# Performance work log

Measured on AMD Instinct MI355X. Metric: run time of the kernel, lower is better.

## Reference

```python
import jax, jax.numpy as jnp
import numpy as np

KERNEL_MUL = 2.0
KERNEL_NUM = 5


def _mmd(source, target):
    b = source.shape[0]
    total = jnp.concatenate([source, target], axis=0)  # [2N, D]
    # ||a-b||^2 = ||a||^2 + ||b||^2 - 2 a.b  (GEMM form, avoids [2N,2N,D])
    sq = jnp.sum(total * total, axis=1)  # [2N]
    l2 = sq[:, None] + sq[None, :] - 2.0 * (total @ total.T)  # [2N, 2N]
    n = total.shape[0]
    # bandwidth computed on detached distances (torch uses .data)
    bandwidth = jax.lax.stop_gradient(jnp.sum(l2)) / (n * n - n)
    kernels = sum(jnp.exp(-l2 / (bandwidth * KERNEL_MUL ** i)) for i in range(KERNEL_NUM))
    xx = kernels[:b, :b]
    yy = kernels[b:, b:]
    xy = kernels[:b, b:]
    yx = kernels[b:, :b]
    return jnp.mean(xx + yy - xy - yx)


def setup_inputs() -> dict:
    key = jax.random.key(0)
    k1, k2 = jax.random.split(key)
    source = jax.random.normal(k1, (4096, 512), dtype=jnp.float32)
    target = jax.random.normal(k2, (4096, 512), dtype=jnp.float32)
    return {"source": source, "target": target}


def reference(source, target):
    return _mmd(source, target)
```

## Files before the change

### kernel.cpp

```cpp
#include <hip/hip_runtime.h>
#include <stdint.h>

typedef signed char s8;
typedef int i32x4 __attribute__((ext_vector_type(4)));

#define B_HALF 4096
#define NROWS 8192
#define DCOL 512
#define BM 128
#define TT 64
#define NTILES 2080
#define KT 8
#define QSCALE 32.0f
#define INV_S2 (1.0f / 1024.0f)
#define PREP_BLOCKS (NROWS / 16)
#define NREP 8

__global__ void zero_kernel(uint4* __restrict__ p) {
  int t = threadIdx.x;
#pragma unroll
  for (int i = 0; i < 5; ++i)
    p[t + i * 256] = (uint4){0u, 0u, 0u, 0u};
}

__global__ __launch_bounds__(256) void prep_kernel(const float* __restrict__ src,
    const float* __restrict__ tgt, s8* __restrict__ qp,
    float* __restrict__ sqq, float* __restrict__ colsum_rep,
    double* __restrict__ sumsq_rep, unsigned int* __restrict__ counter,
    float* __restrict__ gf_out) {
  __shared__ float cs[4][DCOL];
  __shared__ double redd[4];
  __shared__ int lastFlag;
  int tid = threadIdx.x;
  int lane = tid & 63, wid = tid >> 6;
  float cpart[8] = {0.f,0.f,0.f,0.f,0.f,0.f,0.f,0.f};
  float myssq = 0.f;
  int row0 = blockIdx.x * 16;
#pragma unroll
  for (int r = 0; r < 4; ++r) {
    int row = row0 + r * 4 + wid;
    const float* x = (row < B_HALF) ? (src + (size_t)row * DCOL)
                                    : (tgt + (size_t)(row - B_HALF) * DCOL);
    float4 v0 = *reinterpret_cast<const float4*>(x + lane * 8);
    float4 v1 = *reinterpret_cast<const float4*>(x + lane * 8 + 4);
    float vals[8] = {v0.x, v0.y, v0.z, v0.w, v1.x, v1.y, v1.z, v1.w};
    union { s8 c[8]; uint2 u; } pu;
    int iq = 0;
#pragma unroll
    for (int q = 0; q < 8; ++q) {
      float f = vals[q];
      myssq += f * f;
      cpart[q] += f;
      int k = __float2int_rn(fminf(fmaxf(f * QSCALE, -127.f), 127.f));
      pu.c[q] = (s8)k;
      iq += k * k;
    }
    *reinterpret_cast<uint2*>(qp + (size_t)row * DCOL + lane * 8) = pu.u;
#pragma unroll
    for (int o = 32; o > 0; o >>= 1) iq += __shfl_down(iq, o);
    if (lane == 0) sqq[row] = (float)iq * INV_S2;
  }
  double dssq = (double)myssq;
#pragma unroll
  for (int o = 32; o > 0; o >>= 1) dssq += __shfl_down(dssq, o);
  if (lane == 0) redd[wid] = dssq;
#pragma unroll
  for (int q = 0; q < 8; ++q) cs[wid][lane * 8 + q] = cpart[q];
  __syncthreads();
  int rep = (blockIdx.x & (NREP - 1)) * DCOL;
  int c = tid;
  atomicAdd(&colsum_rep[rep + c],
            cs[0][c] + cs[1][c] + cs[2][c] + cs[3][c]);
  atomicAdd(&colsum_rep[rep + c + 256],
            cs[0][c + 256] + cs[1][c + 256] + cs[2][c + 256] + cs[3][c + 256]);
  if (tid == 0)
    atomicAdd(&sumsq_rep[blockIdx.x & (NREP - 1)],
              redd[0] + redd[1] + redd[2] + redd[3]);

  asm volatile("s_waitcnt vmcnt(0)" ::: "memory");
  __syncthreads();
  if (tid == 0)
    lastFlag = ((atomicAdd(counter, 1u) % (unsigned)PREP_BLOCKS) == PREP_BLOCKS - 1);
  __syncthreads();
  if (lastFlag) {
    float c0 = 0.f, c1 = 0.f;
#pragma unroll
    for (int r = 0; r < NREP; ++r) {
      c0 += atomicAdd(&colsum_rep[r * DCOL + tid], 0.f);
      c1 += atomicAdd(&colsum_rep[r * DCOL + tid + 256], 0.f);
    }
    double scs = (double)c0 * c0 + (double)c1 * c1;
#pragma unroll
    for (int o = 32; o > 0; o >>= 1) scs += __shfl_down(scs, o);
    if (lane == 0) redd[wid] = scs;
    __syncthreads();
    if (tid == 0) {
      double C2 = redd[0] + redd[1] + redd[2] + redd[3];
      double S = 0.0;
#pragma unroll
      for (int r = 0; r < NREP; ++r) S += atomicAdd(&sumsq_rep[r], 0.0);
      double n = (double)NROWS;
      double bwv = (2.0 * n * S - 2.0 * C2) / (n * n - n);
      gf_out[0] = (float)(-1.0 / (16.0 * bwv));
    }
  }
}

#define GLDS(gptr, lptr) __builtin_amdgcn_global_load_lds( \
    (const __attribute__((address_space(1))) void*)(gptr), \
    (__attribute__((address_space(3))) void*)(lptr), 16, 0, 0)

#define STAGE(KT_, BUF_) do { \
    GLDS(gA0 + (size_t)(KT_) * 64,             &qA[BUF_][wid * 2048]); \
    GLDS(gA0 + (size_t)(KT_) * 64 + 16 * DCOL, &qA[BUF_][wid * 2048 + 1024]); \
    GLDS(gB0 + (size_t)(KT_) * 64,             &qB[BUF_][wid * 2048]); \
    GLDS(gB0 + (size_t)(KT_) * 64 + 16 * DCOL, &qB[BUF_][wid * 2048 + 1024]); \
  } while (0)

__global__ __launch_bounds__(256, 3) void mmd_gemm_kernel(
    const s8* __restrict__ qp, const float* __restrict__ sqq,
    const float* __restrict__ gf_ptr, float* __restrict__ partials) {
  __shared__ __align__(16) s8 qA[3][8192];
  __shared__ __align__(16) s8 qB[3][8192];
  __shared__ float sqR[BM], sqC[BM];

  int bid = blockIdx.x;
  int t6 = (bid & 7) * (NTILES / 8) + (bid >> 3);
  int I = 0, rem = t6;
  while (rem >= TT - I) { rem -= TT - I; ++I; }
  int J = I + rem;
  int rowStart = I * BM, colStart = J * BM;

  int tid = threadIdx.x;
  int lane = tid & 63, wid = tid >> 6;
  int wr = wid >> 1, wc = wid & 1;
  int r15 = lane & 15, kg = lane >> 4;

  int u = (lane & 7) ^ (lane >> 3);
  int drow0 = wid * 16 + (lane >> 3);
  const s8* gA0 = qp + (size_t)(rowStart + drow0 * 2 + (u >> 2)) * DCOL + (u & 3) * 16;
  const s8* gB0 = qp + (size_t)(colStart + drow0 * 2 + (u >> 2)) * DCOL + (u & 3) * 16;

  int laneOff = ((r15 >> 1) * 128) +
                (((((r15 & 1) << 2) | kg) ^ ((r15 >> 1) & 7)) << 4);
  int aBase = wr * 4096 + laneOff;
  int bBase = wc * 4096 + laneOff;

  STAGE(0, 0);
  STAGE(1, 1);
  if (tid < BM) sqR[tid] = sqq[rowStart + tid];
  else          sqC[tid - BM] = sqq[colStart + (tid - BM)];
  float gf = gf_ptr[0];
  asm volatile("s_waitcnt vmcnt(4) lgkmcnt(0)" ::: "memory");
  __builtin_amdgcn_s_barrier();

  i32x4 acc[4][4];
#pragma unroll
  for (int m = 0; m < 4; ++m)
#pragma unroll
    for (int n = 0; n < 4; ++n) acc[m][n] = (i32x4){0, 0, 0, 0};

#pragma unroll
  for (int kt = 0; kt < KT; ++kt) {
    const int buf = kt % 3;

    i32x4 a[4], b[4];
#pragma unroll
    for (int m = 0; m < 4; ++m)
      a[m] = *reinterpret_cast<const i32x4*>(&qA[buf][aBase + m * 1024]);
#pragma unroll
    for (int n = 0; n < 4; ++n)
      b[n] = *reinterpret_cast<const i32x4*>(&qB[buf][bBase + n * 1024]);

    if (kt + 2 < KT) STAGE(kt + 2, (kt + 2) % 3);

#pragma unroll
    for (int m = 0; m < 4; ++m)
#pragma unroll
      for (int n = 0; n < 4; ++n)
        acc[m][n] = __builtin_amdgcn_mfma_i32_16x16x64_i8(a[m], b[n], acc[m][n], 0, 0, 0);

    if (kt + 2 < KT) {
      asm volatile("s_waitcnt vmcnt(4)" ::: "memory");
      __builtin_amdgcn_s_barrier();
    } else if (kt + 1 < KT) {
      asm volatile("s_waitcnt vmcnt(0)" ::: "memory");
      __builtin_amdgcn_s_barrier();
    }
  }

  float partial = 0.f;
  int rbase = (lane >> 4) * 4;
#pragma unroll
  for (int m = 0; m < 4; ++m) {
    float sr[4];
#pragma unroll
    for (int e = 0; e < 4; ++e) sr[e] = sqR[wr * 64 + m * 16 + rbase + e];
#pragma unroll
    for (int n = 0; n < 4; ++n) {
      float sc = sqC[wc * 64 + n * 16 + r15];
#pragma unroll
      for (int e = 0; e < 4; ++e) {
        float d = (float)acc[m][n][e] * INV_S2;
        float l2v = sr[e] + sc - 2.f * d;
        float uu = __expf(gf * l2v);
        float u2 = uu * uu, u4 = u2 * u2, u8 = u4 * u4, u16v = u8 * u8;
        partial += uu + u2 + u4 + u8 + u16v;
      }
    }
  }
  float wsign = ((I == J) ? 1.f : 2.f) *
                (((rowStart < B_HALF) == (colStart < B_HALF)) ? 1.f : -1.f);
  partial *= wsign;
#pragma unroll
  for (int o = 32; o > 0; o >>= 1) partial += __shfl_down(partial, o);
  if (lane == 0) partials[bid * 4 + wid] = partial;
}

__global__ void finalize_kernel(const float* __restrict__ partials,
                                float* __restrict__ out) {
  __shared__ double red[256];
  int tid = threadIdx.x;
  double s = 0.0;
  for (int i = tid; i < NTILES * 4; i += 256) s += (double)partials[i];
  red[tid] = s;
  __syncthreads();
  for (int o = 128; o > 0; o >>= 1) {
    if (tid < o) red[tid] += red[tid + o];
    __syncthreads();
  }
  if (tid == 0) out[0] = (float)(red[0] / (4096.0 * 4096.0));
}

extern "C" void kernel_launch(void* const* d_in, const int* in_sizes, int n_in,
                              void* d_out, int out_size, void* d_ws, size_t ws_size,
                              hipStream_t stream) {
  const float* src = (const float*)d_in[0];
  const float* tgt = (const float*)d_in[1];
  char* ws = (char*)d_ws;

  float*        colsum_rep = (float*)(ws + 0);
  double*       sumsq_rep  = (double*)(ws + 16384);
  unsigned int* counter    = (unsigned int*)(ws + 16448);
  float*        gfp        = (float*)(ws + 16452);
  float*        sqq        = (float*)(ws + 20480);
  float*        partials   = (float*)(ws + 53248);
  s8*           qp         = (s8*)(ws + 98304);

  zero_kernel<<<1, 256, 0, stream>>>((uint4*)ws);

  prep_kernel<<<PREP_BLOCKS, 256, 0, stream>>>(src, tgt, qp, sqq, colsum_rep,
                                               sumsq_rep, counter, gfp);
  mmd_gemm_kernel<<<NTILES, 256, 0, stream>>>(qp, sqq, gfp, partials);
  finalize_kernel<<<1, 256, 0, stream>>>(partials, (float*)d_out);
}
```

Measured before the change: 70.26 us.

## Fuse bandwidth reduction into GEMM prologue and final sum into last-block epilogue

Removes the last-block bandwidth computation from the prep kernel. Each GEMM block now recomputes the bandwidth redundantly from the replicated column sums and sum-of-squares. The separate finalize kernel is also dropped: each GEMM block writes its partial to a slot, and the last block to arrive (tracked with an atomic counter) reduces all slots and writes the output. This saves one kernel launch and the serial tail work in prep, at the cost of extra global reads and double-precision work per GEMM block plus an atomic counter and fence at the end of each block.

Result: slower. 114.3 us (+62.6%).

```diff
diff --git a/kernel.cpp b/kernel.cpp
--- a/kernel.cpp
+++ b/kernel.cpp
@@ -26,11 +26,9 @@
 __global__ __launch_bounds__(256) void prep_kernel(const float* __restrict__ src,
     const float* __restrict__ tgt, s8* __restrict__ qp,
     float* __restrict__ sqq, float* __restrict__ colsum_rep,
-    double* __restrict__ sumsq_rep, unsigned int* __restrict__ counter,
-    float* __restrict__ gf_out) {
+    double* __restrict__ sumsq_rep) {
   __shared__ float cs[4][DCOL];
   __shared__ double redd[4];
-  __shared__ int lastFlag;
   int tid = threadIdx.x;
   int lane = tid & 63, wid = tid >> 6;
   float cpart[8] = {0.f,0.f,0.f,0.f,0.f,0.f,0.f,0.f};
@@ -76,34 +74,6 @@
   if (tid == 0)
     atomicAdd(&sumsq_rep[blockIdx.x & (NREP - 1)],
               redd[0] + redd[1] + redd[2] + redd[3]);
-
-  asm volatile("s_waitcnt vmcnt(0)" ::: "memory");
-  __syncthreads();
-  if (tid == 0)
-    lastFlag = ((atomicAdd(counter, 1u) % (unsigned)PREP_BLOCKS) == PREP_BLOCKS - 1);
-  __syncthreads();
-  if (lastFlag) {
-    float c0 = 0.f, c1 = 0.f;
-#pragma unroll
-    for (int r = 0; r < NREP; ++r) {
-      c0 += atomicAdd(&colsum_rep[r * DCOL + tid], 0.f);
-      c1 += atomicAdd(&colsum_rep[r * DCOL + tid + 256], 0.f);
-    }
-    double scs = (double)c0 * c0 + (double)c1 * c1;
-#pragma unroll
-    for (int o = 32; o > 0; o >>= 1) scs += __shfl_down(scs, o);
-    if (lane == 0) redd[wid] = scs;
-    __syncthreads();
-    if (tid == 0) {
-      double C2 = redd[0] + redd[1] + redd[2] + redd[3];
-      double S = 0.0;
-#pragma unroll
-      for (int r = 0; r < NREP; ++r) S += atomicAdd(&sumsq_rep[r], 0.0);
-      double n = (double)NROWS;
-      double bwv = (2.0 * n * S - 2.0 * C2) / (n * n - n);
-      gf_out[0] = (float)(-1.0 / (16.0 * bwv));
-    }
-  }
 }
 
 #define GLDS(gptr, lptr) __builtin_amdgcn_global_load_lds( \
@@ -119,10 +89,17 @@
 
 __global__ __launch_bounds__(256, 3) void mmd_gemm_kernel(
     const s8* __restrict__ qp, const float* __restrict__ sqq,
-    const float* __restrict__ gf_ptr, float* __restrict__ partials) {
+    const float* __restrict__ colsum_rep, const double* __restrict__ sumsq_rep,
+    float* __restrict__ slots, unsigned int* __restrict__ counter,
+    float* __restrict__ out) {
   __shared__ __align__(16) s8 qA[3][8192];
   __shared__ __align__(16) s8 qB[3][8192];
   __shared__ float sqR[BM], sqC[BM];
+  __shared__ double redd[4];
+  __shared__ double sS;
+  __shared__ float sGf;
+  __shared__ float wpart[4];
+  __shared__ int isLast;
 
   int bid = blockIdx.x;
   int t6 = (bid & 7) * (NTILES / 8) + (bid >> 3);
@@ -150,9 +127,33 @@
   STAGE(1, 1);
   if (tid < BM) sqR[tid] = sqq[rowStart + tid];
   else          sqC[tid - BM] = sqq[colStart + (tid - BM)];
-  float gf = gf_ptr[0];
+
+  double sld = (wid == 0 && lane < NREP) ? sumsq_rep[lane] : 0.0;
+  float c0 = 0.f, c1 = 0.f;
+#pragma unroll
+  for (int r = 0; r < NREP; ++r) {
+    c0 += colsum_rep[r * DCOL + tid];
+    c1 += colsum_rep[r * DCOL + tid + 256];
+  }
+  double scs = (double)c0 * c0 + (double)c1 * c1;
+#pragma unroll
+  for (int o = 32; o > 0; o >>= 1) scs += __shfl_down(scs, o);
+  if (lane == 0) redd[wid] = scs;
+  if (wid == 0) {
+#pragma unroll
+    for (int o = 4; o > 0; o >>= 1) sld += __shfl_down(sld, o);
+    if (lane == 0) sS = sld;
+  }
+
   asm volatile("s_waitcnt vmcnt(4) lgkmcnt(0)" ::: "memory");
   __builtin_amdgcn_s_barrier();
+
+  if (tid == 0) {
+    double C2 = redd[0] + redd[1] + redd[2] + redd[3];
+    double n = (double)NROWS;
+    double bwv = (2.0 * n * sS - 2.0 * C2) / (n * n - n);
+    sGf = (float)(-1.0 / (16.0 * bwv));
+  }
 
   i32x4 acc[4][4];
 #pragma unroll
@@ -189,6 +190,7 @@
     }
   }
 
+  float gf = sGf;
   float partial = 0.f;
   int rbase = (lane >> 4) * 4;
 #pragma unroll
@@ -214,22 +216,29 @@
   partial *= wsign;
 #pragma unroll
   for (int o = 32; o > 0; o >>= 1) partial += __shfl_down(partial, o);
-  if (lane == 0) partials[bid * 4 + wid] = partial;
-}
-
-__global__ void finalize_kernel(const float* __restrict__ partials,
-                                float* __restrict__ out) {
-  __shared__ double red[256];
-  int tid = threadIdx.x;
-  double s = 0.0;
-  for (int i = tid; i < NTILES * 4; i += 256) s += (double)partials[i];
-  red[tid] = s;
-  __syncthreads();
-  for (int o = 128; o > 0; o >>= 1) {
-    if (tid < o) red[tid] += red[tid + o];
+  if (lane == 0) wpart[wid] = partial;
+  __syncthreads();
+
+  if (tid == 0) {
+    float bp = wpart[0] + wpart[1] + wpart[2] + wpart[3];
+    atomicExch(&slots[bid], bp);
+  }
+  asm volatile("s_waitcnt vmcnt(0)" ::: "memory");
+  __syncthreads();
+  if (tid == 0)
+    isLast = ((atomicAdd(counter, 1u) % (unsigned)NTILES) == NTILES - 1);
+  __syncthreads();
+  if (isLast) {
+    double s = 0.0;
+    for (int i = tid; i < NTILES; i += 256)
+      s += (double)atomicAdd(&slots[i], 0.f);
+#pragma unroll
+    for (int o = 32; o > 0; o >>= 1) s += __shfl_down(s, o);
+    if (lane == 0) redd[wid] = s;
     __syncthreads();
-  }
-  if (tid == 0) out[0] = (float)(red[0] / (4096.0 * 4096.0));
+    if (tid == 0)
+      out[0] = (float)((redd[0] + redd[1] + redd[2] + redd[3]) / (4096.0 * 4096.0));
+  }
 }
 
 extern "C" void kernel_launch(void* const* d_in, const int* in_sizes, int n_in,
@@ -242,15 +251,14 @@
   float*        colsum_rep = (float*)(ws + 0);
   double*       sumsq_rep  = (double*)(ws + 16384);
   unsigned int* counter    = (unsigned int*)(ws + 16448);
-  float*        gfp        = (float*)(ws + 16452);
   float*        sqq        = (float*)(ws + 20480);
-  float*        partials   = (float*)(ws + 53248);
+  float*        slots      = (float*)(ws + 53248);
   s8*           qp         = (s8*)(ws + 98304);
 
   zero_kernel<<<1, 256, 0, stream>>>((uint4*)ws);
 
-  prep_kernel<<<PREP_BLOCKS, 256, 0, stream>>>(src, tgt, qp, sqq, colsum_rep,
-                                               sumsq_rep, counter, gfp);
-  mmd_gemm_kernel<<<NTILES, 256, 0, stream>>>(qp, sqq, gfp, partials);
-  finalize_kernel<<<1, 256, 0, stream>>>(partials, (float*)d_out);
-}
+  prep_kernel<<<PREP_BLOCKS, 256, 0, stream>>>(src, tgt, qp, sqq,
+                                               colsum_rep, sumsq_rep);
+  mmd_gemm_kernel<<<NTILES, 256, 0, stream>>>(qp, sqq, colsum_rep, sumsq_rep,
+                                              slots, counter, (float*)d_out);
+}
```
